# Kernel optimization log

Hardware: AMD Instinct MI355X
Metric: run time of the kernel (lower is better)

## Reference

```python
import jax, jax.numpy as jnp
import numpy as np

B, N, P = 8192, 4096, 8
D = N // P  # 512
EPS = 1e-5


def setup_inputs() -> dict:
    key = jax.random.key(0)
    ks = jax.random.split(key, 7)
    bound = 1.0 / np.sqrt(D)
    return {
        "x": jax.random.normal(ks[0], (B, N), dtype=jnp.float32),
        "weights1": jax.random.normal(ks[1], (P, D, D), dtype=jnp.float32) * bound,
        "bias1": jax.random.uniform(ks[2], (N,), jnp.float32, -bound, bound),
        "weights2": jax.random.normal(ks[3], (P, D, D), dtype=jnp.float32) * bound,
        "bias2": jax.random.uniform(ks[4], (N,), jnp.float32, -bound, bound),
        "bn_weight": jnp.ones((N,), jnp.float32),
        "bn_bias": jnp.zeros((N,), jnp.float32),
        "gamma3": jax.random.normal(ks[5], (N,), jnp.float32) * 0.1,
        "beta3": jax.random.normal(ks[6], (N,), jnp.float32) * 0.1,
    }


def _block_matmul(x, w):
    # x: [B, N], w: [P, D, D] -> equivalent to x @ block_diag(*w)
    b = x.shape[0]
    return jnp.einsum("bpd,pde->bpe", x.reshape(b, P, D), w).reshape(b, N)


def reference(x, weights1, bias1, weights2, bias2, bn_weight, bn_bias, gamma3, beta3):
    h = _block_matmul(x, weights1) + bias1  # [B, N]
    # BatchNorm1d in training mode: biased batch statistics over the batch axis
    mean = jnp.mean(h, axis=0)
    var = jnp.mean((h - mean) ** 2, axis=0)
    o1 = (h - mean) * jax.lax.rsqrt(var + EPS) * bn_weight + bn_bias
    o3 = _block_matmul(o1, weights2) + bias2 + x  # residual
    # sigmoid-gated activation: (gamma + sigmoid(beta*x)*(1-gamma)) * x
    o4 = (gamma3 + jax.nn.sigmoid(beta3 * o3) * (1.0 - gamma3)) * o3
    return o4
```

## Files before the change

### kernel.cpp

```cpp
#include <hip/hip_runtime.h>
#include <hip/hip_bf16.h>
#include <cstdint>
#include <cstddef>

#define B_ROWS 8192
#define N_COLS 4096
#define P_BLK 8
#define D_BLK 512
#define EPSV 1e-5f

typedef __bf16 bf16x8 __attribute__((ext_vector_type(8)));
typedef float f32x4 __attribute__((ext_vector_type(4)));

__device__ __forceinline__ void async_ld16(const void* g, void* l) {
    __builtin_amdgcn_global_load_lds(
        (const __attribute__((address_space(1))) void*)g,
        (__attribute__((address_space(3))) void*)l,
        16, 0, 0);
}

__global__ __launch_bounds__(256) void cvt_x_k(const float* __restrict__ x,
                                               __hip_bfloat16* __restrict__ xb) {
    size_t i = ((size_t)blockIdx.x * 256 + threadIdx.x) * 8;
    float4 v0 = *(const float4*)(x + i);
    float4 v1 = *(const float4*)(x + i + 4);
    union { __hip_bfloat16 h[8]; uint4 u; } r;
    r.h[0] = __float2bfloat16(v0.x); r.h[1] = __float2bfloat16(v0.y);
    r.h[2] = __float2bfloat16(v0.z); r.h[3] = __float2bfloat16(v0.w);
    r.h[4] = __float2bfloat16(v1.x); r.h[5] = __float2bfloat16(v1.y);
    r.h[6] = __float2bfloat16(v1.z); r.h[7] = __float2bfloat16(v1.w);
    *(uint4*)(xb + i) = r.u;
}

__global__ __launch_bounds__(256) void tr_w_k(const float* __restrict__ W,
                                              const float* __restrict__ scale,
                                              __hip_bfloat16* __restrict__ Wt) {
    __shared__ float t[32][33];
    int p = blockIdx.z;
    int d0 = blockIdx.x * 32, e0 = blockIdx.y * 32;
    const float* Wp = W + (size_t)p * D_BLK * D_BLK;
    for (int j = 0; j < 32; j += 8) {
        int d = d0 + threadIdx.y + j;
        float v = Wp[(size_t)d * D_BLK + e0 + threadIdx.x];
        if (scale) v *= scale[p * D_BLK + d];
        t[threadIdx.y + j][threadIdx.x] = v;
    }
    __syncthreads();
    __hip_bfloat16* Wtp = Wt + (size_t)p * D_BLK * D_BLK;
    for (int j = 0; j < 32; j += 8) {
        int e = e0 + threadIdx.y + j;
        Wtp[(size_t)e * D_BLK + d0 + threadIdx.x] =
            __float2bfloat16(t[threadIdx.x][threadIdx.y + j]);
    }
}

__global__ __launch_bounds__(256) void finalize_k(const float* __restrict__ sum,
                                                  const float* __restrict__ sumsq,
                                                  const float* __restrict__ bnw,
                                                  const float* __restrict__ bnb,
                                                  float* __restrict__ a,
                                                  float* __restrict__ c) {
    int i = blockIdx.x * 256 + threadIdx.x;
    float m = sum[i] * (1.0f / B_ROWS);
    float var = sumsq[i] * (1.0f / B_ROWS) - m * m;
    float ai = bnw[i] * rsqrtf(var + EPSV);
    a[i] = ai;
    c[i] = bnb[i] - m * ai;
}

__global__ __launch_bounds__(256) void bias2p_k(const float* __restrict__ W2,
                                                const float* __restrict__ c,
                                                const float* __restrict__ bias2,
                                                float* __restrict__ out) {
    int col = blockIdx.x * 256 + threadIdx.x;
    int p = col >> 9;
    int e = col & (D_BLK - 1);
    const float* Wp = W2 + (size_t)p * D_BLK * D_BLK + e;
    const float* cp = c + p * D_BLK;
    float acc = 0.0f;
    for (int d = 0; d < D_BLK; d++) acc += cp[d] * Wp[(size_t)d * D_BLK];
    out[col] = bias2[col] + acc;
}

__device__ __forceinline__ void gemm_core(const __hip_bfloat16* __restrict__ A,
                                          const __hip_bfloat16* __restrict__ Bt,
                                          f32x4 acc[4][4]) {
    __shared__ __hip_bfloat16 As[128 * 32];
    __shared__ __hip_bfloat16 Bs[128 * 32];

    const int tid = threadIdx.x;
    const int lane = tid & 63;
    const int wave = tid >> 6;
    const int wm = (wave >> 1) * 64;
    const int wn = (wave & 1) * 64;
    const int row_base = blockIdx.x * 128;
    const int col_base = blockIdx.y * 128;
    const int p = col_base >> 9;
    const int ebase = col_base & (D_BLK - 1);

    const int ar = tid >> 2;
    const int kp = (tid & 3) * 8;
    const __hip_bfloat16* a_src0 = A + (size_t)(row_base + ar) * N_COLS + p * D_BLK + kp;
    const __hip_bfloat16* a_src1 = a_src0 + (size_t)64 * N_COLS;
    const __hip_bfloat16* b_src0 = Bt + (size_t)(p * D_BLK + ebase + ar) * D_BLK + kp;
    const __hip_bfloat16* b_src1 = b_src0 + (size_t)64 * D_BLK;
    __hip_bfloat16* a_dst0 = &As[ar * 32 + kp];
    __hip_bfloat16* a_dst1 = &As[(ar + 64) * 32 + kp];
    __hip_bfloat16* b_dst0 = &Bs[ar * 32 + kp];
    __hip_bfloat16* b_dst1 = &Bs[(ar + 64) * 32 + kp];

    const int fm = lane & 15;
    const int fkoff = (lane >> 4) * 8;

    for (int i = 0; i < 4; i++)
        for (int j = 0; j < 4; j++)
            acc[i][j] = (f32x4){0.0f, 0.0f, 0.0f, 0.0f};

    for (int k0 = 0; k0 < D_BLK; k0 += 32) {
        async_ld16(a_src0, a_dst0);
        async_ld16(a_src1, a_dst1);
        async_ld16(b_src0, b_dst0);
        async_ld16(b_src1, b_dst1);
        a_src0 += 32; a_src1 += 32; b_src0 += 32; b_src1 += 32;
        __syncthreads();

        bf16x8 af[4], bfr[4];
#pragma unroll
        for (int i = 0; i < 4; i++)
            af[i] = *(const bf16x8*)&As[(wm + i * 16 + fm) * 32 + fkoff];
#pragma unroll
        for (int j = 0; j < 4; j++)
            bfr[j] = *(const bf16x8*)&Bs[(wn + j * 16 + fm) * 32 + fkoff];
#pragma unroll
        for (int i = 0; i < 4; i++)
#pragma unroll
            for (int j = 0; j < 4; j++)
                acc[i][j] = __builtin_amdgcn_mfma_f32_16x16x32_bf16(
                    af[i], bfr[j], acc[i][j], 0, 0, 0);
        __syncthreads();
    }
}

__global__ __launch_bounds__(256) void gemm1_k(const __hip_bfloat16* __restrict__ xb,
                                               const __hip_bfloat16* __restrict__ w1t,
                                               const float* __restrict__ bias1,
                                               __hip_bfloat16* __restrict__ h,
                                               float* __restrict__ sum,
                                               float* __restrict__ sumsq) {
    f32x4 acc[4][4];
    gemm_core(xb, w1t, acc);

    const int tid = threadIdx.x;
    const int lane = tid & 63;
    const int wave = tid >> 6;
    const int wm = (wave >> 1) * 64;
    const int wn = (wave & 1) * 64;
    const int row_base = blockIdx.x * 128;
    const int col_base = blockIdx.y * 128;
    const int cr = (lane >> 4) * 4;
    const int cc = lane & 15;

#pragma unroll
    for (int j = 0; j < 4; j++) {
        const int col = col_base + wn + j * 16 + cc;
        const float b1 = bias1[col];
        float s = 0.0f, sq = 0.0f;
#pragma unroll
        for (int i = 0; i < 4; i++) {
            const int row0 = row_base + wm + i * 16 + cr;
#pragma unroll
            for (int r = 0; r < 4; r++) {
                float v = acc[i][j][r] + b1;
                h[(size_t)(row0 + r) * N_COLS + col] = __float2bfloat16(v);
                s += v;
                sq += v * v;
            }
        }
        s  += __shfl_xor(s, 16);  s  += __shfl_xor(s, 32);
        sq += __shfl_xor(sq, 16); sq += __shfl_xor(sq, 32);
        if (lane < 16) {
            atomicAdd(&sum[col], s);
            atomicAdd(&sumsq[col], sq);
        }
    }
}

__global__ __launch_bounds__(256) void gemm2_k(const __hip_bfloat16* __restrict__ h,
                                               const __hip_bfloat16* __restrict__ w2t,
                                               const float* __restrict__ bias2p,
                                               const float* __restrict__ x,
                                               const float* __restrict__ gamma3,
                                               const float* __restrict__ beta3,
                                               float* __restrict__ out) {
    f32x4 acc[4][4];
    gemm_core(h, w2t, acc);

    const int tid = threadIdx.x;
    const int lane = tid & 63;
    const int wave = tid >> 6;
    const int wm = (wave >> 1) * 64;
    const int wn = (wave & 1) * 64;
    const int row_base = blockIdx.x * 128;
    const int col_base = blockIdx.y * 128;
    const int cr = (lane >> 4) * 4;
    const int cc = lane & 15;

#pragma unroll
    for (int j = 0; j < 4; j++) {
        const int col = col_base + wn + j * 16 + cc;
        const float bb = bias2p[col];
        const float g  = gamma3[col];
        const float be = beta3[col];
#pragma unroll
        for (int i = 0; i < 4; i++) {
            const int row0 = row_base + wm + i * 16 + cr;
#pragma unroll
            for (int r = 0; r < 4; r++) {
                const size_t idx = (size_t)(row0 + r) * N_COLS + col;
                float o3 = acc[i][j][r] + bb + x[idx];
                float sg = 1.0f / (1.0f + expf(-be * o3));
                out[idx] = (g + sg * (1.0f - g)) * o3;
            }
        }
    }
}

extern "C" void kernel_launch(void* const* d_in, const int* in_sizes, int n_in,
                              void* d_out, int out_size, void* d_ws, size_t ws_size,
                              hipStream_t stream) {
    const float* x     = (const float*)d_in[0];
    const float* W1    = (const float*)d_in[1];
    const float* bias1 = (const float*)d_in[2];
    const float* W2    = (const float*)d_in[3];
    const float* bias2 = (const float*)d_in[4];
    const float* bnw   = (const float*)d_in[5];
    const float* bnb   = (const float*)d_in[6];
    const float* gam3  = (const float*)d_in[7];
    const float* bet3  = (const float*)d_in[8];
    float* out = (float*)d_out;

    char* ws = (char*)d_ws;
    const size_t XB_BYTES = (size_t)B_ROWS * N_COLS * 2;
    const size_t H_BYTES  = (size_t)B_ROWS * N_COLS * 2;
    const size_t WT_BYTES = (size_t)P_BLK * D_BLK * D_BLK * 2;
    const size_t V_BYTES  = (size_t)N_COLS * 4;

    __hip_bfloat16* xb   = (__hip_bfloat16*)(ws);
    __hip_bfloat16* hbuf = (__hip_bfloat16*)(ws + XB_BYTES);
    __hip_bfloat16* w1t  = (__hip_bfloat16*)(ws + XB_BYTES + H_BYTES);
    __hip_bfloat16* w2t  = (__hip_bfloat16*)(ws + XB_BYTES + H_BYTES + WT_BYTES);
    float* sums  = (float*)(ws + XB_BYTES + H_BYTES + 2 * WT_BYTES);
    float* sumsq = (float*)((char*)sums + V_BYTES);
    float* a_sc  = (float*)((char*)sums + 2 * V_BYTES);
    float* c_sh  = (float*)((char*)sums + 3 * V_BYTES);
    float* b2p   = (float*)((char*)sums + 4 * V_BYTES);

    (void)in_sizes; (void)n_in; (void)out_size; (void)ws_size;

    hipMemsetAsync(sums, 0, 2 * V_BYTES, stream);

    cvt_x_k<<<dim3((B_ROWS * N_COLS) / (256 * 8)), dim3(256), 0, stream>>>(x, xb);
    tr_w_k<<<dim3(16, 16, 8), dim3(32, 8), 0, stream>>>(W1, nullptr, w1t);
    gemm1_k<<<dim3(B_ROWS / 128, N_COLS / 128), dim3(256), 0, stream>>>(
        xb, w1t, bias1, hbuf, sums, sumsq);
    finalize_k<<<dim3(N_COLS / 256), dim3(256), 0, stream>>>(sums, sumsq, bnw, bnb, a_sc, c_sh);
    tr_w_k<<<dim3(16, 16, 8), dim3(32, 8), 0, stream>>>(W2, a_sc, w2t);
    bias2p_k<<<dim3(N_COLS / 256), dim3(256), 0, stream>>>(W2, c_sh, bias2, b2p);
    gemm2_k<<<dim3(B_ROWS / 128, N_COLS / 128), dim3(256), 0, stream>>>(
        hbuf, w2t, b2p, x, gam3, bet3, out);
}
```

Baseline: 463.9 us.

## Swizzle LDS tiles, remap tile order for L2 reuse, read residual as bf16

Applies an XOR swizzle to the k-chunks of the shared-memory A/B tiles to reduce LDS bank conflicts on MFMA fragment reads. Replaces the 2D grid with a 1D grid decoded into a grouped tile order so blocks sharing a row tile run together and reuse it from L2. The gemm2 epilogue reads the residual from the bf16 copy of x instead of fp32 x, halving that traffic at the cost of residual precision.

New measurement: 402.3 us. 1.15x faster.

```diff
diff --git a/kernel.cpp b/kernel.cpp
--- a/kernel.cpp
+++ b/kernel.cpp
@@ -17,6 +17,13 @@
         (const __attribute__((address_space(1))) void*)g,
         (__attribute__((address_space(3))) void*)l,
         16, 0, 0);
+}
+
+__device__ __forceinline__ void decode_tile(int n, int& row_base, int& col_base) {
+    const int row_tile = n >> 5;
+    const int col_tile = ((n & 7) << 2) | ((n >> 3) & 3);
+    row_base = row_tile * 128;
+    col_base = col_tile * 128;
 }
 
 __global__ __launch_bounds__(256) void cvt_x_k(const float* __restrict__ x,
@@ -84,6 +91,7 @@
 
 __device__ __forceinline__ void gemm_core(const __hip_bfloat16* __restrict__ A,
                                           const __hip_bfloat16* __restrict__ Bt,
+                                          int row_base, int col_base,
                                           f32x4 acc[4][4]) {
     __shared__ __hip_bfloat16 As[128 * 32];
     __shared__ __hip_bfloat16 Bs[128 * 32];
@@ -93,24 +101,25 @@
     const int wave = tid >> 6;
     const int wm = (wave >> 1) * 64;
     const int wn = (wave & 1) * 64;
-    const int row_base = blockIdx.x * 128;
-    const int col_base = blockIdx.y * 128;
     const int p = col_base >> 9;
     const int ebase = col_base & (D_BLK - 1);
 
     const int ar = tid >> 2;
-    const int kp = (tid & 3) * 8;
-    const __hip_bfloat16* a_src0 = A + (size_t)(row_base + ar) * N_COLS + p * D_BLK + kp;
+    const int c4 = tid & 3;
+    const int kq8 = (c4 ^ ((tid >> 3) & 3)) * 8;
+    const int dst_off = ar * 32 + c4 * 8;
+
+    const __hip_bfloat16* a_src0 = A + (size_t)(row_base + ar) * N_COLS + p * D_BLK + kq8;
     const __hip_bfloat16* a_src1 = a_src0 + (size_t)64 * N_COLS;
-    const __hip_bfloat16* b_src0 = Bt + (size_t)(p * D_BLK + ebase + ar) * D_BLK + kp;
+    const __hip_bfloat16* b_src0 = Bt + (size_t)(p * D_BLK + ebase + ar) * D_BLK + kq8;
     const __hip_bfloat16* b_src1 = b_src0 + (size_t)64 * D_BLK;
-    __hip_bfloat16* a_dst0 = &As[ar * 32 + kp];
-    __hip_bfloat16* a_dst1 = &As[(ar + 64) * 32 + kp];
-    __hip_bfloat16* b_dst0 = &Bs[ar * 32 + kp];
-    __hip_bfloat16* b_dst1 = &Bs[(ar + 64) * 32 + kp];
+    __hip_bfloat16* a_dst0 = &As[dst_off];
+    __hip_bfloat16* a_dst1 = &As[dst_off + 64 * 32];
+    __hip_bfloat16* b_dst0 = &Bs[dst_off];
+    __hip_bfloat16* b_dst1 = &Bs[dst_off + 64 * 32];
 
     const int fm = lane & 15;
-    const int fkoff = (lane >> 4) * 8;
+    const int fkoff = ((lane >> 4) ^ ((fm >> 1) & 3)) * 8;
 
     for (int i = 0; i < 4; i++)
         for (int j = 0; j < 4; j++)
@@ -147,16 +156,17 @@
                                                __hip_bfloat16* __restrict__ h,
                                                float* __restrict__ sum,
                                                float* __restrict__ sumsq) {
+    int row_base, col_base;
+    decode_tile(blockIdx.x, row_base, col_base);
+
     f32x4 acc[4][4];
-    gemm_core(xb, w1t, acc);
+    gemm_core(xb, w1t, row_base, col_base, acc);
 
     const int tid = threadIdx.x;
     const int lane = tid & 63;
     const int wave = tid >> 6;
     const int wm = (wave >> 1) * 64;
     const int wn = (wave & 1) * 64;
-    const int row_base = blockIdx.x * 128;
-    const int col_base = blockIdx.y * 128;
     const int cr = (lane >> 4) * 4;
     const int cc = lane & 15;
 
@@ -188,20 +198,21 @@
 __global__ __launch_bounds__(256) void gemm2_k(const __hip_bfloat16* __restrict__ h,
                                                const __hip_bfloat16* __restrict__ w2t,
                                                const float* __restrict__ bias2p,
-                                               const float* __restrict__ x,
+                                               const __hip_bfloat16* __restrict__ xb,
                                                const float* __restrict__ gamma3,
                                                const float* __restrict__ beta3,
                                                float* __restrict__ out) {
+    int row_base, col_base;
+    decode_tile(blockIdx.x, row_base, col_base);
+
     f32x4 acc[4][4];
-    gemm_core(h, w2t, acc);
+    gemm_core(h, w2t, row_base, col_base, acc);
 
     const int tid = threadIdx.x;
     const int lane = tid & 63;
     const int wave = tid >> 6;
     const int wm = (wave >> 1) * 64;
     const int wn = (wave & 1) * 64;
-    const int row_base = blockIdx.x * 128;
-    const int col_base = blockIdx.y * 128;
     const int cr = (lane >> 4) * 4;
     const int cc = lane & 15;
 
@@ -217,7 +228,7 @@
 #pragma unroll
             for (int r = 0; r < 4; r++) {
                 const size_t idx = (size_t)(row0 + r) * N_COLS + col;
-                float o3 = acc[i][j][r] + bb + x[idx];
+                float o3 = acc[i][j][r] + bb + __bfloat162float(xb[idx]);
                 float sg = 1.0f / (1.0f + expf(-be * o3));
                 out[idx] = (g + sg * (1.0f - g)) * o3;
             }
@@ -261,11 +272,11 @@
 
     cvt_x_k<<<dim3((B_ROWS * N_COLS) / (256 * 8)), dim3(256), 0, stream>>>(x, xb);
     tr_w_k<<<dim3(16, 16, 8), dim3(32, 8), 0, stream>>>(W1, nullptr, w1t);
-    gemm1_k<<<dim3(B_ROWS / 128, N_COLS / 128), dim3(256), 0, stream>>>(
+    gemm1_k<<<dim3((B_ROWS / 128) * (N_COLS / 128)), dim3(256), 0, stream>>>(
         xb, w1t, bias1, hbuf, sums, sumsq);
     finalize_k<<<dim3(N_COLS / 256), dim3(256), 0, stream>>>(sums, sumsq, bnw, bnb, a_sc, c_sh);
     tr_w_k<<<dim3(16, 16, 8), dim3(32, 8), 0, stream>>>(W2, a_sc, w2t);
     bias2p_k<<<dim3(N_COLS / 256), dim3(256), 0, stream>>>(W2, c_sh, bias2, b2p);
-    gemm2_k<<<dim3(B_ROWS / 128, N_COLS / 128), dim3(256), 0, stream>>>(
-        hbuf, w2t, b2p, x, gam3, bet3, out);
-}
+    gemm2_k<<<dim3((B_ROWS / 128) * (N_COLS / 128)), dim3(256), 0, stream>>>(
+        hbuf, w2t, b2p, xb, gam3, bet3, out);
+}
```
